# Performance work log

Measured on AMD Instinct MI355X. Metric: run time of the kernel, lower is better.

The kernel has to match this reference:

```python
import jax, jax.numpy as jnp
import numpy as np

K, T, F = 12000, 35, 7          # voxels, points-per-voxel (cfg.VOXEL_POINT_COUNT), point feature dim
B, D, H, W = 1, 10, 400, 352    # scatter grid: [batch, depth, cfg.INPUT_HEIGHT, cfg.INPUT_WIDTH]
C_OUT = 128
EPS = 1e-3                      # Keras BatchNormalization default epsilon


def setup_inputs() -> dict:
    key = jax.random.key(0)
    ks = jax.random.split(key, 20)
    # point features, with per-voxel padding (points beyond count are zero)
    feat = jax.random.normal(ks[0], (K, T, F), dtype=jnp.float32)
    counts = jax.random.randint(ks[1], (K,), 1, T + 1)
    valid = (jnp.arange(T)[None, :] < counts[:, None]).astype(jnp.float32)  # [K,T]
    feat = feat * valid[:, :, None]
    # voxel coordinates: (batch, d, h, w), in-range per dimension
    c0 = jax.random.randint(ks[2], (K,), 0, B)
    c1 = jax.random.randint(ks[3], (K,), 0, D)
    c2 = jax.random.randint(ks[4], (K,), 0, H)
    c3 = jax.random.randint(ks[5], (K,), 0, W)
    coordinate = jnp.stack([c0, c1, c2, c3], axis=1).astype(jnp.int32)  # [K,4]
    p = lambda i, shape: jax.random.normal(ks[i], shape, dtype=jnp.float32) * 0.1
    return {
        "input_feature": feat,
        "w1": p(6, (F, 16)), "b1": p(7, (16,)),
        "gamma1": 1.0 + p(8, (16,)), "beta1": p(9, (16,)),
        "mean1": p(10, (16,)), "var1": jax.random.uniform(ks[11], (16,), minval=0.5, maxval=1.5),
        "w2": p(12, (32, 64)), "b2": p(13, (64,)),
        "gamma2": 1.0 + p(14, (64,)), "beta2": p(15, (64,)),
        "mean2": p(16, (64,)), "var2": jax.random.uniform(ks[17], (64,), minval=0.5, maxval=1.5),
        "coordinate": coordinate,
        "batch_size": B,
    }


def vfe(x, mask, w, b, gamma, beta, mean, var):
    # Dense + relu (per point), inference BatchNorm, max-aggregate, tile-concat, mask
    dense = jax.nn.relu(jnp.einsum('ktf,fu->ktu', x, w) + b)
    pw = gamma * (dense - mean) * jax.lax.rsqrt(var + EPS) + beta  # [K,T,U]
    agg = jnp.max(pw, axis=1, keepdims=True)                       # [K,1,U]
    cat = jnp.concatenate([pw, jnp.broadcast_to(agg, pw.shape)], axis=2)  # [K,T,2U]
    return cat * mask


def reference(input_feature, w1, b1, gamma1, beta1, mean1, var1,
              w2, b2, gamma2, beta2, mean2, var2, coordinate, batch_size):
    # mask: point is valid if max over its features != 0
    mask = (jnp.max(input_feature, axis=2, keepdims=True) != 0).astype(input_feature.dtype)
    x = vfe(input_feature, mask, w1, b1, gamma1, beta1, mean1, var1)   # [K,T,32]
    x = vfe(x, mask, w2, b2, gamma2, beta2, mean2, var2)               # [K,T,128]
    voxelwise = jnp.max(x, axis=1)                                     # [K,128]
    out = jnp.zeros((batch_size, D, H, W, C_OUT), dtype=voxelwise.dtype)
    # tf.scatter_nd semantics: duplicate indices accumulate (add)
    out = out.at[coordinate[:, 0], coordinate[:, 1], coordinate[:, 2], coordinate[:, 3]].add(voxelwise)
    return out
```

## Files before the change

### kernel.cpp

```cpp
#include <hip/hip_runtime.h>

#define KVOX 12000
#define TPTS 35
#define FIN  7
#define DD   10
#define HH   400
#define WW   352
#define CO   128
#define EPSBN 1e-3f
#define NCELL (DD * HH * WW)
#define CB    3000
#define TOTALF4 ((size_t)NCELL * 32)
#define SB    1500

static_assert(CB * 4 == KVOX, "grid covers voxels exactly");

__global__ __launch_bounds__(256) void fused_fill_compute(
    const float* __restrict__ feat,
    const float* __restrict__ w1, const float* __restrict__ b1,
    const float* __restrict__ g1, const float* __restrict__ be1,
    const float* __restrict__ m1, const float* __restrict__ v1,
    const float* __restrict__ w2, const float* __restrict__ b2,
    const float* __restrict__ g2, const float* __restrict__ be2,
    const float* __restrict__ m2, const float* __restrict__ v2,
    float* __restrict__ vox,
    float* __restrict__ out)
{
    const int tid  = threadIdx.x;
    const int wv   = tid >> 6;
    const int lane = tid & 63;
    const int k    = blockIdx.x * 4 + wv;

    __shared__ __align__(16) float sxp[4][TPTS][8];
    __shared__ __align__(16) float spwm[4][TPTS][16];
    __shared__ __align__(16) float sagg[4][16];

    const bool fillFirst = (blockIdx.x & 1);

    auto do_fill = [&]() {
        const float4 z = make_float4(0.f, 0.f, 0.f, 0.f);
        float4* o4 = (float4*)out;
        const size_t stride = (size_t)CB * 256;
        for (size_t i = (size_t)blockIdx.x * 256 + tid; i < TOTALF4; i += stride)
            o4[i] = z;
    };

    if (fillFirst) do_fill();

    const float* fk = feat + (size_t)k * (TPTS * FIN);

    for (int i = lane; i < TPTS * FIN; i += 64)
        sxp[wv][i / FIN][i % FIN] = fk[i];
    if (lane < TPTS) sxp[wv][lane][FIN] = 0.0f;

    bool pred = false;
    if (lane < TPTS) {
        const float* row = fk + lane * FIN;
        float mx = row[0];
        #pragma unroll
        for (int f = 1; f < FIN; ++f) mx = fmaxf(mx, row[f]);
        pred = (mx != 0.0f);
    }
    const unsigned long long bal = __ballot(pred);
    const int nvalid = __popcll(bal);
    __syncthreads();

    if (lane < 16) {
        const int u = lane;
        float w1c[8];
        #pragma unroll
        for (int f = 0; f < FIN; ++f) w1c[f] = w1[f * 16 + u];
        w1c[FIN] = 0.0f;
        const float b     = b1[u];
        const float scale = g1[u] * rsqrtf(v1[u] + EPSBN);
        const float shift = be1[u] - m1[u] * scale;

        float agg = -INFINITY;
        float pw[TPTS];
        #pragma unroll
        for (int t = 0; t < TPTS; ++t) {
            const float4 xa = *(const float4*)&sxp[wv][t][0];
            const float4 xb = *(const float4*)&sxp[wv][t][4];
            float d = b;
            d = fmaf(xa.x, w1c[0], d); d = fmaf(xa.y, w1c[1], d);
            d = fmaf(xa.z, w1c[2], d); d = fmaf(xa.w, w1c[3], d);
            d = fmaf(xb.x, w1c[4], d); d = fmaf(xb.y, w1c[5], d);
            d = fmaf(xb.z, w1c[6], d); d = fmaf(xb.w, w1c[7], d);
            d = fmaxf(d, 0.0f);
            const float p = fmaf(d, scale, shift);
            agg = fmaxf(agg, p);
            pw[t] = p;
        }
        sagg[wv][u] = agg;
        #pragma unroll
        for (int t = 0; t < TPTS; ++t) {
            const float mk = ((bal >> t) & 1ULL) ? 1.0f : 0.0f;
            spwm[wv][t][u] = pw[t] * mk;
        }
    }
    __syncthreads();

    {
        const int v = lane;
        float w2c[32];
        #pragma unroll
        for (int u = 0; u < 32; ++u) w2c[u] = w2[u * 64 + v];
        const float b     = b2[v];
        const float scale = g2[v] * rsqrtf(v2[v] + EPSBN);
        const float shift = be2[v] - m2[v] * scale;

        float aggdot = 0.0f;
        {
            const float4* ar = (const float4*)&sagg[wv][0];
            #pragma unroll
            for (int q = 0; q < 4; ++q) {
                const float4 a = ar[q];
                aggdot = fmaf(a.x, w2c[16 + 4 * q + 0], aggdot);
                aggdot = fmaf(a.y, w2c[16 + 4 * q + 1], aggdot);
                aggdot = fmaf(a.z, w2c[16 + 4 * q + 2], aggdot);
                aggdot = fmaf(a.w, w2c[16 + 4 * q + 3], aggdot);
            }
        }

        float aggAll = -INFINITY;
        float voxA   = -INFINITY;
        #pragma unroll 7
        for (int t = 0; t < TPTS; ++t) {
            const float mk = ((bal >> t) & 1ULL) ? 1.0f : 0.0f;
            const float4* xr = (const float4*)&spwm[wv][t][0];
            float d = fmaf(mk, aggdot, b);
            #pragma unroll
            for (int q = 0; q < 4; ++q) {
                const float4 xv = xr[q];
                d = fmaf(xv.x, w2c[4 * q + 0], d);
                d = fmaf(xv.y, w2c[4 * q + 1], d);
                d = fmaf(xv.z, w2c[4 * q + 2], d);
                d = fmaf(xv.w, w2c[4 * q + 3], d);
            }
            d = fmaxf(d, 0.0f);
            const float p = fmaf(d, scale, shift);
            aggAll = fmaxf(aggAll, p);
            voxA   = fmaxf(voxA, p * mk);
        }
        float voxB;
        if (nvalid == 0)          voxB = 0.0f;
        else if (nvalid < TPTS)   voxB = fmaxf(aggAll, 0.0f);
        else                      voxB = aggAll;

        float* vk = vox + (size_t)k * CO;
        vk[v]      = voxA;
        vk[64 + v] = voxB;
    }

    if (!fillFirst) do_fill();
}

__global__ __launch_bounds__(256) void scatter_add(
    const float* __restrict__ vox, const int* __restrict__ coord,
    float* __restrict__ out)
{
    const int stride = SB * 256;
    for (int i = blockIdx.x * 256 + threadIdx.x; i < KVOX * CO; i += stride) {
        const int k  = i >> 7;
        const int ch = i & (CO - 1);
        const int4 c = ((const int4*)coord)[k];
        const int loc = (((c.x * DD + c.y) * HH + c.z) * WW + c.w);
        atomicAdd(out + (size_t)loc * CO + ch, vox[i]);
    }
}

__global__ __launch_bounds__(64) void vfe_scatter_atomic(
    const float* __restrict__ feat,
    const float* __restrict__ w1, const float* __restrict__ b1,
    const float* __restrict__ g1, const float* __restrict__ be1,
    const float* __restrict__ m1, const float* __restrict__ v1,
    const float* __restrict__ w2, const float* __restrict__ b2,
    const float* __restrict__ g2, const float* __restrict__ be2,
    const float* __restrict__ m2, const float* __restrict__ v2,
    const int* __restrict__ coord,
    float* __restrict__ out)
{
    const int k   = blockIdx.x;
    const int tid = threadIdx.x;
    __shared__ float sx[TPTS][FIN];
    __shared__ float smask[TPTS];
    __shared__ __align__(16) float sx2[TPTS][32];
    const float* fk = feat + (size_t)k * (TPTS * FIN);
    for (int i = tid; i < TPTS * FIN; i += 64) ((float*)sx)[i] = fk[i];
    __syncthreads();
    bool pred = false;
    if (tid < TPTS) {
        float mx = sx[tid][0];
        #pragma unroll
        for (int f = 1; f < FIN; ++f) mx = fmaxf(mx, sx[tid][f]);
        pred = (mx != 0.0f);
        smask[tid] = pred ? 1.0f : 0.0f;
    }
    unsigned long long bal = __ballot(pred);
    const int nvalid = __popcll(bal);
    __syncthreads();
    if (tid < 16) {
        const int u = tid;
        float w1c[FIN];
        #pragma unroll
        for (int f = 0; f < FIN; ++f) w1c[f] = w1[f * 16 + u];
        const float b = b1[u];
        const float scale = g1[u] * rsqrtf(v1[u] + EPSBN);
        const float shift = be1[u] - m1[u] * scale;
        float agg = -INFINITY;
        float pw[TPTS];
        #pragma unroll
        for (int t = 0; t < TPTS; ++t) {
            float d = b;
            #pragma unroll
            for (int f = 0; f < FIN; ++f) d = fmaf(sx[t][f], w1c[f], d);
            d = fmaxf(d, 0.0f);
            float p = fmaf(d, scale, shift);
            agg = fmaxf(agg, p);
            pw[t] = p;
        }
        #pragma unroll
        for (int t = 0; t < TPTS; ++t) {
            const float mk = smask[t];
            sx2[t][u] = pw[t] * mk;
            sx2[t][16 + u] = agg * mk;
        }
    }
    __syncthreads();
    {
        const int v = tid;
        float w2c[32];
        #pragma unroll
        for (int u = 0; u < 32; ++u) w2c[u] = w2[u * 64 + v];
        const float b = b2[v];
        const float scale = g2[v] * rsqrtf(v2[v] + EPSBN);
        const float shift = be2[v] - m2[v] * scale;
        float aggAll = -INFINITY, voxA = -INFINITY;
        #pragma unroll 5
        for (int t = 0; t < TPTS; ++t) {
            float d = b;
            const float4* xr = (const float4*)(&sx2[t][0]);
            #pragma unroll
            for (int q = 0; q < 8; ++q) {
                float4 xv = xr[q];
                d = fmaf(xv.x, w2c[4 * q + 0], d);
                d = fmaf(xv.y, w2c[4 * q + 1], d);
                d = fmaf(xv.z, w2c[4 * q + 2], d);
                d = fmaf(xv.w, w2c[4 * q + 3], d);
            }
            d = fmaxf(d, 0.0f);
            float p = fmaf(d, scale, shift);
            aggAll = fmaxf(aggAll, p);
            voxA = fmaxf(voxA, p * smask[t]);
        }
        float voxB;
        if (nvalid == 0) voxB = 0.0f;
        else if (nvalid < TPTS) voxB = fmaxf(aggAll, 0.0f);
        else voxB = aggAll;
        const int4 c = ((const int4*)coord)[k];
        const int loc = (((c.x * DD + c.y) * HH + c.z) * WW + c.w);
        float* o = out + (size_t)loc * CO;
        atomicAdd(o + v, voxA);
        atomicAdd(o + 64 + v, voxB);
    }
}

extern "C" void kernel_launch(void* const* d_in, const int* in_sizes, int n_in,
                              void* d_out, int out_size, void* d_ws, size_t ws_size,
                              hipStream_t stream) {
    const float* feat = (const float*)d_in[0];
    const float* w1   = (const float*)d_in[1];
    const float* b1   = (const float*)d_in[2];
    const float* g1   = (const float*)d_in[3];
    const float* be1  = (const float*)d_in[4];
    const float* m1   = (const float*)d_in[5];
    const float* v1   = (const float*)d_in[6];
    const float* w2   = (const float*)d_in[7];
    const float* b2   = (const float*)d_in[8];
    const float* g2   = (const float*)d_in[9];
    const float* be2  = (const float*)d_in[10];
    const float* m2   = (const float*)d_in[11];
    const float* v2   = (const float*)d_in[12];
    const int*   coord = (const int*)d_in[13];
    float* out = (float*)d_out;

    const size_t voxB = (size_t)KVOX * CO * sizeof(float);

    if (ws_size >= voxB) {
        float* vox = (float*)d_ws;
        fused_fill_compute<<<CB, 256, 0, stream>>>(feat, w1, b1, g1, be1, m1, v1,
                                                   w2, b2, g2, be2, m2, v2,
                                                   vox, out);
        scatter_add<<<SB, 256, 0, stream>>>(vox, coord, out);
    } else {
        hipMemsetAsync(d_out, 0, (size_t)out_size * sizeof(float), stream);
        vfe_scatter_atomic<<<KVOX, 64, 0, stream>>>(feat, w1, b1, g1, be1, m1, v1,
                                                    w2, b2, g2, be2, m2, v2, coord, out);
    }
}
```

Before: 749.3 us.

## Split zero-fill into own kernel and fuse scatter atomics into VFE compute

```diff
diff --git a/kernel.cpp b/kernel.cpp
--- a/kernel.cpp
+++ b/kernel.cpp
@@ -9,13 +9,21 @@
 #define CO   128
 #define EPSBN 1e-3f
 #define NCELL (DD * HH * WW)
+#define TOTALF4 ((size_t)NCELL * 32)
+#define FILLB 2048
 #define CB    3000
-#define TOTALF4 ((size_t)NCELL * 32)
-#define SB    1500
 
 static_assert(CB * 4 == KVOX, "grid covers voxels exactly");
 
-__global__ __launch_bounds__(256) void fused_fill_compute(
+__global__ __launch_bounds__(256) void fill_out(float4* __restrict__ o4)
+{
+    const float4 z = make_float4(0.f, 0.f, 0.f, 0.f);
+    const size_t stride = (size_t)FILLB * 256;
+    for (size_t i = (size_t)blockIdx.x * 256 + threadIdx.x; i < TOTALF4; i += stride)
+        o4[i] = z;
+}
+
+__global__ __launch_bounds__(256) void vfe_scatter(
     const float* __restrict__ feat,
     const float* __restrict__ w1, const float* __restrict__ b1,
     const float* __restrict__ g1, const float* __restrict__ be1,
@@ -23,7 +31,7 @@
     const float* __restrict__ w2, const float* __restrict__ b2,
     const float* __restrict__ g2, const float* __restrict__ be2,
     const float* __restrict__ m2, const float* __restrict__ v2,
-    float* __restrict__ vox,
+    const int* __restrict__ coord,
     float* __restrict__ out)
 {
     const int tid  = threadIdx.x;
@@ -34,18 +42,6 @@
     __shared__ __align__(16) float sxp[4][TPTS][8];
     __shared__ __align__(16) float spwm[4][TPTS][16];
     __shared__ __align__(16) float sagg[4][16];
-
-    const bool fillFirst = (blockIdx.x & 1);
-
-    auto do_fill = [&]() {
-        const float4 z = make_float4(0.f, 0.f, 0.f, 0.f);
-        float4* o4 = (float4*)out;
-        const size_t stride = (size_t)CB * 256;
-        for (size_t i = (size_t)blockIdx.x * 256 + tid; i < TOTALF4; i += stride)
-            o4[i] = z;
-    };
-
-    if (fillFirst) do_fill();
 
     const float* fk = feat + (size_t)k * (TPTS * FIN);
 
@@ -147,120 +143,10 @@
         else if (nvalid < TPTS)   voxB = fmaxf(aggAll, 0.0f);
         else                      voxB = aggAll;
 
-        float* vk = vox + (size_t)k * CO;
-        vk[v]      = voxA;
-        vk[64 + v] = voxB;
-    }
-
-    if (!fillFirst) do_fill();
-}
-
-__global__ __launch_bounds__(256) void scatter_add(
-    const float* __restrict__ vox, const int* __restrict__ coord,
-    float* __restrict__ out)
-{
-    const int stride = SB * 256;
-    for (int i = blockIdx.x * 256 + threadIdx.x; i < KVOX * CO; i += stride) {
-        const int k  = i >> 7;
-        const int ch = i & (CO - 1);
-        const int4 c = ((const int4*)coord)[k];
-        const int loc = (((c.x * DD + c.y) * HH + c.z) * WW + c.w);
-        atomicAdd(out + (size_t)loc * CO + ch, vox[i]);
-    }
-}
-
-__global__ __launch_bounds__(64) void vfe_scatter_atomic(
-    const float* __restrict__ feat,
-    const float* __restrict__ w1, const float* __restrict__ b1,
-    const float* __restrict__ g1, const float* __restrict__ be1,
-    const float* __restrict__ m1, const float* __restrict__ v1,
-    const float* __restrict__ w2, const float* __restrict__ b2,
-    const float* __restrict__ g2, const float* __restrict__ be2,
-    const float* __restrict__ m2, const float* __restrict__ v2,
-    const int* __restrict__ coord,
-    float* __restrict__ out)
-{
-    const int k   = blockIdx.x;
-    const int tid = threadIdx.x;
-    __shared__ float sx[TPTS][FIN];
-    __shared__ float smask[TPTS];
-    __shared__ __align__(16) float sx2[TPTS][32];
-    const float* fk = feat + (size_t)k * (TPTS * FIN);
-    for (int i = tid; i < TPTS * FIN; i += 64) ((float*)sx)[i] = fk[i];
-    __syncthreads();
-    bool pred = false;
-    if (tid < TPTS) {
-        float mx = sx[tid][0];
-        #pragma unroll
-        for (int f = 1; f < FIN; ++f) mx = fmaxf(mx, sx[tid][f]);
-        pred = (mx != 0.0f);
-        smask[tid] = pred ? 1.0f : 0.0f;
-    }
-    unsigned long long bal = __ballot(pred);
-    const int nvalid = __popcll(bal);
-    __syncthreads();
-    if (tid < 16) {
-        const int u = tid;
-        float w1c[FIN];
-        #pragma unroll
-        for (int f = 0; f < FIN; ++f) w1c[f] = w1[f * 16 + u];
-        const float b = b1[u];
-        const float scale = g1[u] * rsqrtf(v1[u] + EPSBN);
-        const float shift = be1[u] - m1[u] * scale;
-        float agg = -INFINITY;
-        float pw[TPTS];
-        #pragma unroll
-        for (int t = 0; t < TPTS; ++t) {
-            float d = b;
-            #pragma unroll
-            for (int f = 0; f < FIN; ++f) d = fmaf(sx[t][f], w1c[f], d);
-            d = fmaxf(d, 0.0f);
-            float p = fmaf(d, scale, shift);
-            agg = fmaxf(agg, p);
-            pw[t] = p;
-        }
-        #pragma unroll
-        for (int t = 0; t < TPTS; ++t) {
-            const float mk = smask[t];
-            sx2[t][u] = pw[t] * mk;
-            sx2[t][16 + u] = agg * mk;
-        }
-    }
-    __syncthreads();
-    {
-        const int v = tid;
-        float w2c[32];
-        #pragma unroll
-        for (int u = 0; u < 32; ++u) w2c[u] = w2[u * 64 + v];
-        const float b = b2[v];
-        const float scale = g2[v] * rsqrtf(v2[v] + EPSBN);
-        const float shift = be2[v] - m2[v] * scale;
-        float aggAll = -INFINITY, voxA = -INFINITY;
-        #pragma unroll 5
-        for (int t = 0; t < TPTS; ++t) {
-            float d = b;
-            const float4* xr = (const float4*)(&sx2[t][0]);
-            #pragma unroll
-            for (int q = 0; q < 8; ++q) {
-                float4 xv = xr[q];
-                d = fmaf(xv.x, w2c[4 * q + 0], d);
-                d = fmaf(xv.y, w2c[4 * q + 1], d);
-                d = fmaf(xv.z, w2c[4 * q + 2], d);
-                d = fmaf(xv.w, w2c[4 * q + 3], d);
-            }
-            d = fmaxf(d, 0.0f);
-            float p = fmaf(d, scale, shift);
-            aggAll = fmaxf(aggAll, p);
-            voxA = fmaxf(voxA, p * smask[t]);
-        }
-        float voxB;
-        if (nvalid == 0) voxB = 0.0f;
-        else if (nvalid < TPTS) voxB = fmaxf(aggAll, 0.0f);
-        else voxB = aggAll;
         const int4 c = ((const int4*)coord)[k];
         const int loc = (((c.x * DD + c.y) * HH + c.z) * WW + c.w);
         float* o = out + (size_t)loc * CO;
-        atomicAdd(o + v, voxA);
+        atomicAdd(o + v,      voxA);
         atomicAdd(o + 64 + v, voxB);
     }
 }
@@ -284,17 +170,7 @@
     const int*   coord = (const int*)d_in[13];
     float* out = (float*)d_out;
 
-    const size_t voxB = (size_t)KVOX * CO * sizeof(float);
-
-    if (ws_size >= voxB) {
-        float* vox = (float*)d_ws;
-        fused_fill_compute<<<CB, 256, 0, stream>>>(feat, w1, b1, g1, be1, m1, v1,
-                                                   w2, b2, g2, be2, m2, v2,
-                                                   vox, out);
-        scatter_add<<<SB, 256, 0, stream>>>(vox, coord, out);
-    } else {
-        hipMemsetAsync(d_out, 0, (size_t)out_size * sizeof(float), stream);
-        vfe_scatter_atomic<<<KVOX, 64, 0, stream>>>(feat, w1, b1, g1, be1, m1, v1,
-                                                    w2, b2, g2, be2, m2, v2, coord, out);
-    }
+    fill_out<<<FILLB, 256, 0, stream>>>((float4*)out);
+    vfe_scatter<<<CB, 256, 0, stream>>>(feat, w1, b1, g1, be1, m1, v1,
+                                        w2, b2, g2, be2, m2, v2, coord, out);
 }
```

Result: slower. 791.4 us (+5.6%).
